# Optimization experiments

Measured on AMD Instinct MI355X. Metric: run time of the kernel, lower is better.

The kernel has to match this reference:

```python
import jax, jax.numpy as jnp
import numpy as np

N = 50000
E = 640000
H = 128

def setup_inputs() -> dict:
    key = jax.random.key(0)
    ks = jax.random.split(key, 12)
    def lin(kw, fan_in, fan_out):
        # torch nn.Linear default init: U(-1/sqrt(fan_in), 1/sqrt(fan_in))
        lim = 1.0 / np.sqrt(fan_in)
        return jax.random.uniform(kw, (fan_in, fan_out), jnp.float32, -lim, lim)
    def bias(kb, fan_in, fan_out):
        lim = 1.0 / np.sqrt(fan_in)
        return jax.random.uniform(kb, (fan_out,), jnp.float32, -lim, lim)
    return {
        "x": jax.random.normal(ks[0], (N, H), jnp.float32),
        "pos": jax.random.normal(ks[1], (N, 3), jnp.float32),
        "edge_index": jax.random.randint(ks[2], (2, E), 0, N, jnp.int64),
        "msg_w1": lin(ks[3], 2 * H + 1, H), "msg_b1": bias(ks[4], 2 * H + 1, H),
        "msg_w2": lin(ks[5], H, H),         "msg_b2": bias(ks[6], H, H),
        "upd_w1": lin(ks[7], 2 * H, H),     "upd_b1": bias(ks[8], 2 * H, H),
        "upd_w2": lin(ks[9], H, H),         "upd_b2": bias(ks[10], H, H),
    }

def reference(x, pos, edge_index, msg_w1, msg_b1, msg_w2, msg_b2,
              upd_w1, upd_b1, upd_w2, upd_b2):
    send, rec = edge_index[0], edge_index[1]
    # pairwise distance per edge: [E]
    dist = jnp.linalg.norm(pos[send] - pos[rec], axis=1)
    # per-edge state: [E, 2H+1]
    state = jnp.concatenate([x[send], x[rec], dist[:, None]], axis=1)
    # message MLP: Linear -> SiLU -> Linear -> SiLU
    h = jax.nn.silu(state @ msg_w1 + msg_b1)
    message = jax.nn.silu(h @ msg_w2 + msg_b2)  # [E, H]
    # scatter-add into receiving nodes: [N, H]
    aggr = jax.ops.segment_sum(message, rec, num_segments=x.shape[0])
    # update MLP: Linear -> SiLU -> Linear
    u = jax.nn.silu(jnp.concatenate([x, aggr], axis=1) @ upd_w1 + upd_b1)
    update = u @ upd_w2 + upd_b2
    return update
```

## Files before the change

### kernel.cpp

```cpp
#include <hip/hip_runtime.h>
#include <math.h>

#define H 128

typedef unsigned short u16;
typedef unsigned int u32;
typedef __attribute__((ext_vector_type(4))) u32 u32x4;
typedef __attribute__((ext_vector_type(8))) __bf16 bf16x8;
typedef __attribute__((ext_vector_type(4))) float f32x4;
typedef __attribute__((ext_vector_type(16))) float f32x16;

union Frag { u32x4 u; bf16x8 b; };

__device__ __forceinline__ u32 pack2(float lo, float hi) {
    union { __bf16 b[2]; u32 u; } v;
    v.b[0] = (__bf16)lo; v.b[1] = (__bf16)hi;
    return v.u;
}
__device__ __forceinline__ float bflo(u32 w) {
    union { u32 i; float f; } v; v.i = w << 16; return v.f;
}
__device__ __forceinline__ float bfhi(u32 w) {
    union { u32 i; float f; } v; v.i = w & 0xffff0000u; return v.f;
}
__device__ __forceinline__ float silu(float v) {
    float e = __expf(-v);
    return v * __builtin_amdgcn_rcpf(1.0f + e);
}
__device__ __forceinline__ bf16x8 f8frag(float4 lo, float4 hi) {
    Frag f;
    f.u = (u32x4){pack2(lo.x, lo.y), pack2(lo.z, lo.w),
                  pack2(hi.x, hi.y), pack2(hi.z, hi.w)};
    return f.b;
}
__device__ __forceinline__ f32x16 mfma(bf16x8 a, bf16x8 b, f32x16 c) {
    return __builtin_amdgcn_mfma_f32_32x32x16_bf16(a, b, c, 0, 0, 0);
}
__device__ __forceinline__ f32x4 mfma16(bf16x8 a, bf16x8 b, f32x4 c) {
    return __builtin_amdgcn_mfma_f32_16x16x32_bf16(a, b, c, 0, 0, 0);
}
#define DPP_RADD(v, ctrl) \
    (v) += __int_as_float(__builtin_amdgcn_update_dpp(0, __float_as_int(v), (ctrl), 0xf, 0xf, 1))

__global__ void prep_kernel(const float* __restrict__ mw1, const float* __restrict__ mb1,
                            const float* __restrict__ mw2, const float* __restrict__ mb2,
                            const float* __restrict__ uw1, const float* __restrict__ ub1,
                            const float* __restrict__ uw2, const float* __restrict__ ub2,
                            u32* __restrict__ ws) {
    int t = blockIdx.x * blockDim.x + threadIdx.x;
    if (t >= 15936) return;
    if (t >= 15872) {
        int i = t - 15872;
        ws[63488 + i] = pack2(mw1[256 * H + 2 * i], mw1[256 * H + 2 * i + 1]);
        return;
    }
    if (t >= 13312) {
        int slot = t - 13312;
        int lane = slot & 63, fb = slot >> 6;
        int kb = fb >> 3, mt = fb & 7;
        int m = mt * 16 + (lane & 15);
        int quad = lane >> 4;
        u32 out[4];
        #pragma unroll
        for (int p = 0; p < 4; ++p) {
            float v[2];
            #pragma unroll
            for (int h = 0; h < 2; ++h) {
                int k = kb * 32 + quad * 8 + p * 2 + h;
                float val = 0.0f;
                if (k < 128)       val = mw2[(size_t)k * H + m];
                else if (k == 128) val = mb2[m];
                v[h] = val;
            }
            out[p] = pack2(v[0], v[1]);
        }
        u32* dst = ws + 53248 + (size_t)slot * 4;
        dst[0] = out[0]; dst[1] = out[1]; dst[2] = out[2]; dst[3] = out[3];
        return;
    }
    const float *W, *s0, *s1;
    int nK, slot, base;
    if (t < 4352)       { W = mw1; s0 = mw1 + 256 * H; s1 = mb1; nK = 256; slot = t;         base = 0;     }
    else if (t < 6656)  { W = mw2; s0 = mb2; s1 = nullptr;       nK = 128; slot = t - 4352;  base = 17408; }
    else if (t < 11008) { W = uw1; s0 = ub1; s1 = nullptr;       nK = 256; slot = t - 6656;  base = 26624; }
    else                { W = uw2; s0 = ub2; s1 = nullptr;       nK = 128; slot = t - 11008; base = 44032; }
    int lane = slot & 63, fb = slot >> 6;
    int ct, kb;
    if (nK == 256) { ct = fb / 17; kb = fb % 17; }
    else           { ct = fb / 9;  kb = fb % 9;  }
    int m = ct * 32 + (lane & 31);
    int q = lane >> 5;
    u32 out[4];
    #pragma unroll
    for (int p = 0; p < 4; ++p) {
        float v[2];
        #pragma unroll
        for (int h = 0; h < 2; ++h) {
            int k = kb * 16 + q * 8 + p * 2 + h;
            float val = 0.0f;
            if (k < nK)            val = W[(size_t)k * H + m];
            else if (k == nK)      val = s0 ? s0[m] : 0.0f;
            else if (k == nK + 1)  val = s1 ? s1[m] : 0.0f;
            v[h] = val;
        }
        out[p] = pack2(v[0], v[1]);
    }
    u32* dst = ws + base + (size_t)slot * 4;
    dst[0] = out[0]; dst[1] = out[1]; dst[2] = out[2]; dst[3] = out[3];
}

__global__ __launch_bounds__(256, 2) void front_kernel(
    const float* __restrict__ x, const u32* __restrict__ ws,
    u32* __restrict__ Pb, u32* __restrict__ Qb, u32* __restrict__ Ub,
    const float* __restrict__ pos, const int* __restrict__ ei,
    int* __restrict__ deg, int2* __restrict__ bucket,
    int N, int E, int nIter, int PQB, int BKB)
{
    const int b = blockIdx.x;
    if (b < 3 * PQB) {
        const int job = b / PQB;
        const int bb = b - job * PQB;
        const int kbBase = (job == 1) ? 8 : 0;
        const u32* wt = (job == 2) ? (ws + 26624) : ws;
        u32* outb = (job == 0) ? Pb : ((job == 1) ? Qb : Ub);

        const int lane = threadIdx.x & 63;
        const int q = lane >> 5, el = lane & 31;
        const int gw  = bb * 4 + (threadIdx.x >> 6);
        const int gws = PQB * 4;

        for (int it = gw; it < nIter; it += gws) {
            const int nA = it * 32 + el;
            const int ncA = (nA < N) ? nA : (N - 1);
            const float* xA = x + (size_t)ncA * H;

            f32x16 acc[4];
            #pragma unroll
            for (int ct = 0; ct < 4; ++ct) acc[ct] = (f32x16)0.0f;

            #pragma unroll
            for (int kb = 0; kb < 8; ++kb) {
                const int f = kb * 16 + q * 8;
                bf16x8 bA = f8frag(*(const float4*)(xA + f), *(const float4*)(xA + f + 4));
                #pragma unroll
                for (int ct = 0; ct < 4; ++ct) {
                    Frag a; a.u = *(const u32x4*)&wt[((size_t)(ct * 17 + kbBase + kb) * 64 + lane) * 4];
                    acc[ct] = mfma(a.b, bA, acc[ct]);
                }
            }
            if (job == 1) {
                Frag bp; bp.u = (u32x4){0, 0, 0, 0};
                if (q == 0) bp.u.x = pack2(0.0f, 1.0f);
                #pragma unroll
                for (int ct = 0; ct < 4; ++ct) {
                    Frag a; a.u = *(const u32x4*)&ws[((size_t)(ct * 17 + 16) * 64 + lane) * 4];
                    acc[ct] = mfma(a.b, bp.b, acc[ct]);
                }
            }
            if (nA < N) {
                u32* prow = outb + (size_t)nA * 64;
                #pragma unroll
                for (int ct = 0; ct < 4; ++ct)
                    #pragma unroll
                    for (int g = 0; g < 4; ++g) {
                        u32 a = pack2(acc[ct][4*g + 0], acc[ct][4*g + 1]);
                        u32 bb2 = pack2(acc[ct][4*g + 2], acc[ct][4*g + 3]);
                        *(uint2*)(prow + ct * 16 + 4 * g + 2 * q) = make_uint2(a, bb2);
                    }
            }
        }
    } else {
        const int bb = b - 3 * PQB;
        for (int e = bb * 256 + (int)threadIdx.x; e < E; e += BKB * 256) {
            const int s = ei[e];
            const int r = ei[E + e];
            const float dx = pos[s*3]   - pos[r*3];
            const float dy = pos[s*3+1] - pos[r*3+1];
            const float dz = pos[s*3+2] - pos[r*3+2];
            const float dist = sqrtf(dx*dx + dy*dy + dz*dz);
            int slot = atomicAdd(&deg[r], 1);
            if (slot < 64) bucket[(size_t)r * 64 + slot] = make_int2(s, __float_as_int(dist));
        }
    }
}

__global__ __launch_bounds__(256, 3) void aggregate_kernel(
    const u32* __restrict__ Pbf, const u32* __restrict__ Qbf,
    const u32* __restrict__ wdp, const u32* __restrict__ ws16,
    const float* __restrict__ mb2,
    const int* __restrict__ deg, const int2* __restrict__ bucket,
    u32* __restrict__ aggrp, int N)
{
    __shared__ u32x4 af[2048];
    __shared__ float b2s[128];
    __shared__ u32x4 wds[16];
    for (int i = threadIdx.x; i < 2048; i += 256) af[i] = ((const u32x4*)ws16)[i];
    for (int i = threadIdx.x; i < 128; i += 256) b2s[i] = mb2[i];
    if (threadIdx.x < 16) wds[threadIdx.x] = ((const u32x4*)wdp)[threadIdx.x];
    __syncthreads();

    const int lane = threadIdx.x & 63;
    const int quad = lane >> 4, col = lane & 15;

    const int gw  = blockIdx.x * 4 + (threadIdx.x >> 6);
    const int gws = gridDim.x * 4;

    for (int n = gw; n < N; n += gws) {
        int dn = deg[n]; dn = (dn > 64) ? 64 : dn;
        const int nt = (dn + 15) >> 4;
        const u32x4* Qrow = (const u32x4*)(Qbf + (size_t)n * 64);

        f32x4 sum[8];
        #pragma unroll
        for (int mt = 0; mt < 8; ++mt) sum[mt] = (f32x4){0.f, 0.f, 0.f, 0.f};

        for (int t = 0; t < nt; ++t) {
            const int eIdx = t * 16 + col;
            const bool valid = eIdx < dn;
            const int eC = valid ? eIdx : (dn - 1);
            const int2 rec = bucket[(size_t)n * 64 + eC];
            const u32x4* Prow = (const u32x4*)(Pbf + (size_t)rec.x * 64);
            const float dist = __int_as_float(rec.y);

            f32x4 acc[8];
            #pragma unroll
            for (int mt = 0; mt < 8; ++mt)
                acc[mt] = *(const f32x4*)&b2s[mt * 16 + quad * 4];

            #pragma unroll 2
            for (int kb = 0; kb < 4; ++kb) {
                const u32x4 pc = Prow[kb * 4 + quad];
                const u32x4 qc = Qrow[kb * 4 + quad];
                const u32x4 wc = wds[kb * 4 + quad];
                const float v0 = silu(bflo(pc.x) + bflo(qc.x) + dist * bflo(wc.x));
                const float v1 = silu(bfhi(pc.x) + bfhi(qc.x) + dist * bfhi(wc.x));
                const float v2 = silu(bflo(pc.y) + bflo(qc.y) + dist * bflo(wc.y));
                const float v3 = silu(bfhi(pc.y) + bfhi(qc.y) + dist * bfhi(wc.y));
                const float v4 = silu(bflo(pc.z) + bflo(qc.z) + dist * bflo(wc.z));
                const float v5 = silu(bfhi(pc.z) + bfhi(qc.z) + dist * bfhi(wc.z));
                const float v6 = silu(bflo(pc.w) + bflo(qc.w) + dist * bflo(wc.w));
                const float v7 = silu(bfhi(pc.w) + bfhi(qc.w) + dist * bfhi(wc.w));
                Frag bf;
                bf.u = (u32x4){pack2(v0, v1), pack2(v2, v3), pack2(v4, v5), pack2(v6, v7)};
                if (!valid) bf.u = (u32x4){0, 0, 0, 0};
                #pragma unroll
                for (int mt = 0; mt < 8; ++mt) {
                    Frag a; a.u = af[(kb * 8 + mt) * 64 + lane];
                    acc[mt] = mfma16(a.b, bf.b, acc[mt]);
                }
            }
            #pragma unroll
            for (int mt = 0; mt < 8; ++mt) {
                sum[mt][0] += valid ? silu(acc[mt][0]) : 0.0f;
                sum[mt][1] += valid ? silu(acc[mt][1]) : 0.0f;
                sum[mt][2] += valid ? silu(acc[mt][2]) : 0.0f;
                sum[mt][3] += valid ? silu(acc[mt][3]) : 0.0f;
            }
        }

        #pragma unroll
        for (int mt = 0; mt < 8; ++mt)
            #pragma unroll
            for (int r = 0; r < 4; ++r) {
                float v = sum[mt][r];
                DPP_RADD(v, 0x128);
                DPP_RADD(v, 0x124);
                DPP_RADD(v, 0x122);
                DPP_RADD(v, 0x121);
                sum[mt][r] = v;
            }
        if (col == 0) {
            u32* orow = aggrp + (size_t)n * 64;
            #pragma unroll
            for (int mt = 0; mt < 8; ++mt) {
                u32 a = pack2(sum[mt][0], sum[mt][1]);
                u32 b = pack2(sum[mt][2], sum[mt][3]);
                *(uint2*)(orow + mt * 8 + quad * 2) = make_uint2(a, b);
            }
        }
    }
}

__global__ __launch_bounds__(256, 2) void node1_slim(
    const u32* __restrict__ aggrp, const u32* __restrict__ Ub,
    const u32* __restrict__ ws, u32* __restrict__ Hb, int N, int nIter)
{
    __shared__ u32 lds[8192];
    const u32* wsl1 = ws + 26624;
    {
        const u32x4* src = (const u32x4*)wsl1;
        u32x4* dst = (u32x4*)lds;
        for (int i = threadIdx.x; i < 2048; i += 256) {
            int ln = i & 63, fb = i >> 6, ct = fb >> 3, kb = fb & 7;
            dst[i] = src[(ct * 17 + 8 + kb) * 64 + ln];
        }
    }
    __syncthreads();

    const int lane = threadIdx.x & 63;
    const int q = lane >> 5, el = lane & 31;
    const int gw  = blockIdx.x * 4 + (threadIdx.x >> 6);
    const int gws = gridDim.x * 4;

    for (int it = gw; it < nIter; it += gws) {
        const int nA = it * 32 + el;
        const int ncA = (nA < N) ? nA : (N - 1);
        const u32* arow = aggrp + (size_t)ncA * 64;
        const u32* Urow = Ub + (size_t)ncA * 64;

        f32x16 acc[4];
        #pragma unroll
        for (int ct = 0; ct < 4; ++ct) acc[ct] = (f32x16)0.0f;

        #pragma unroll
        for (int kb = 0; kb < 8; ++kb) {
            Frag hb; hb.u = *(const u32x4*)&arow[kb * 8 + q * 4];
            #pragma unroll
            for (int ct = 0; ct < 4; ++ct) {
                Frag a; a.u = *(const u32x4*)&lds[((ct * 8 + kb) * 64 + lane) * 4];
                acc[ct] = mfma(a.b, hb.b, acc[ct]);
            }
        }
        {
            Frag bp; bp.u = (u32x4){0,0,0,0};
            if (q == 0) bp.u.x = 0x00003F80u;
            #pragma unroll
            for (int ct = 0; ct < 4; ++ct) {
                Frag a; a.u = *(const u32x4*)&wsl1[((size_t)(ct * 17 + 16) * 64 + lane) * 4];
                acc[ct] = mfma(a.b, bp.b, acc[ct]);
            }
        }
        if (nA < N) {
            u32* hrow = Hb + (size_t)nA * 64;
            #pragma unroll
            for (int ct = 0; ct < 4; ++ct)
                #pragma unroll
                for (int g = 0; g < 4; ++g) {
                    uint2 uv = *(const uint2*)&Urow[ct * 16 + 4 * g + 2 * q];
                    u32 a = pack2(silu(acc[ct][4*g + 0] + bflo(uv.x)),
                                  silu(acc[ct][4*g + 1] + bfhi(uv.x)));
                    u32 b = pack2(silu(acc[ct][4*g + 2] + bflo(uv.y)),
                                  silu(acc[ct][4*g + 3] + bfhi(uv.y)));
                    *(uint2*)(hrow + ct * 16 + 4 * g + 2 * q) = make_uint2(a, b);
                }
        }
    }
}

__global__ __launch_bounds__(256, 2) void node1_full(
    const float* __restrict__ x, const float* __restrict__ aggr,
    const u32* __restrict__ ws, u32* __restrict__ Hb, int N, int nIter)
{
    __shared__ u32 lds[16384];
    const u32* wsl1 = ws + 26624;
    {
        const u32x4* src = (const u32x4*)wsl1;
        u32x4* dst = (u32x4*)lds;
        for (int i = threadIdx.x; i < 4096; i += 256) {
            int ln = i & 63, fb = i >> 6, ct = fb >> 4, kb = fb & 15;
            dst[i] = src[(ct * 17 + kb) * 64 + ln];
        }
    }
    __syncthreads();

    const int lane = threadIdx.x & 63;
    const int q = lane >> 5, el = lane & 31;
    const int gw  = blockIdx.x * 4 + (threadIdx.x >> 6);
    const int gws = gridDim.x * 4;

    for (int it = gw; it < nIter; it += gws) {
        const int nA = it * 32 + el;
        const int ncA = (nA < N) ? nA : (N - 1);
        const float* xA = x + (size_t)ncA * H;
        const float* gA = aggr + (size_t)ncA * H;

        f32x16 acc[4];
        #pragma unroll
        for (int ct = 0; ct < 4; ++ct) acc[ct] = (f32x16)0.0f;

        #pragma unroll
        for (int kb = 0; kb < 16; ++kb) {
            const int f = kb * 16 + q * 8;
            const float* pA = (f < H) ? (xA + f) : (gA + f - H);
            bf16x8 bA = f8frag(*(const float4*)pA, *(const float4*)(pA + 4));
            #pragma unroll
            for (int ct = 0; ct < 4; ++ct) {
                Frag a; a.u = *(const u32x4*)&lds[((ct * 16 + kb) * 64 + lane) * 4];
                acc[ct] = mfma(a.b, bA, acc[ct]);
            }
        }
        {
            Frag bp; bp.u = (u32x4){0,0,0,0};
            if (q == 0) bp.u.x = 0x00003F80u;
            #pragma unroll
            for (int ct = 0; ct < 4; ++ct) {
                Frag a; a.u = *(const u32x4*)&wsl1[((size_t)(ct * 17 + 16) * 64 + lane) * 4];
                acc[ct] = mfma(a.b, bp.b, acc[ct]);
            }
        }
        if (nA < N) {
            u32* hrow = Hb + (size_t)nA * 64;
            #pragma unroll
            for (int ct = 0; ct < 4; ++ct)
                #pragma unroll
                for (int g = 0; g < 4; ++g) {
                    u32 a = pack2(silu(acc[ct][4*g + 0]), silu(acc[ct][4*g + 1]));
                    u32 b = pack2(silu(acc[ct][4*g + 2]), silu(acc[ct][4*g + 3]));
                    *(uint2*)(hrow + ct * 16 + 4 * g + 2 * q) = make_uint2(a, b);
                }
        }
    }
}

__global__ __launch_bounds__(256, 2) void node2_kernel(
    const u32* __restrict__ Hb, const u32* __restrict__ ws,
    float* __restrict__ out, int N, int nIter)
{
    const u32* wsl2 = ws + 44032;
    const int lane = threadIdx.x & 63;
    const int q = lane >> 5, el = lane & 31;
    const int gw  = blockIdx.x * 4 + (threadIdx.x >> 6);
    const int gws = gridDim.x * 4;

    for (int it = gw; it < nIter; it += gws) {
        const int nA = it * 32 + el;
        const int ncA = (nA < N) ? nA : (N - 1);
        const u32* hrow = Hb + (size_t)ncA * 64;

        f32x16 acc[4];
        #pragma unroll
        for (int ct = 0; ct < 4; ++ct) acc[ct] = (f32x16)0.0f;

        #pragma unroll
        for (int kb = 0; kb < 8; ++kb) {
            Frag hb; hb.u = *(const u32x4*)&hrow[kb * 8 + q * 4];
            #pragma unroll
            for (int ct = 0; ct < 4; ++ct) {
                Frag a; a.u = *(const u32x4*)&wsl2[((size_t)(ct * 9 + kb) * 64 + lane) * 4];
                acc[ct] = mfma(a.b, hb.b, acc[ct]);
            }
        }
        {
            Frag bf; bf.u = (u32x4){0,0,0,0};
            if (q == 0) bf.u.x = 0x00003F80u;
            #pragma unroll
            for (int ct = 0; ct < 4; ++ct) {
                Frag a; a.u = *(const u32x4*)&wsl2[((size_t)(ct * 9 + 8) * 64 + lane) * 4];
                acc[ct] = mfma(a.b, bf.b, acc[ct]);
            }
        }
        if (nA < N) {
            float* orow = out + (size_t)nA * H;
            #pragma unroll
            for (int ct = 0; ct < 4; ++ct)
                #pragma unroll
                for (int g = 0; g < 4; ++g) {
                    float4 v = { acc[ct][4*g + 0], acc[ct][4*g + 1],
                                 acc[ct][4*g + 2], acc[ct][4*g + 3] };
                    *(float4*)(orow + ct * 32 + 8 * g + 4 * q) = v;
                }
        }
    }
}

__global__ __launch_bounds__(256, 2) void edge_mfma(
    const float* __restrict__ x, const float* __restrict__ pos,
    const int* __restrict__ ei, const u32* __restrict__ ws,
    float* __restrict__ aggr, int E, int nIter)
{
    __shared__ u32 lds[16384];
    {
        const u32x4* src = (const u32x4*)ws;
        u32x4* dst = (u32x4*)lds;
        for (int i = threadIdx.x; i < 4096; i += 256) {
            int ln = i & 63, fb = i >> 6, ct = fb >> 4, kb = fb & 15;
            dst[i] = src[(ct * 17 + kb) * 64 + ln];
        }
    }
    __syncthreads();
    const u32* wsl1 = ws;
    const u32* wsl2 = ws + 17408;

    const int lane = threadIdx.x & 63;
    const int q = lane >> 5, el = lane & 31;
    const int gw  = blockIdx.x * 4 + (threadIdx.x >> 6);
    const int gws = gridDim.x * 4;

    for (int it = gw; it < nIter; it += gws) {
        const int e0 = it * 64;
        const int sA = ei[e0 + el],      rA = ei[E + e0 + el];
        const int sB = ei[e0 + 32 + el], rB = ei[E + e0 + 32 + el];
        float dA, dB;
        {
            float ax = pos[sA*3] - pos[rA*3], ay = pos[sA*3+1] - pos[rA*3+1], az = pos[sA*3+2] - pos[rA*3+2];
            dA = sqrtf(ax*ax + ay*ay + az*az);
            float bx = pos[sB*3] - pos[rB*3], by = pos[sB*3+1] - pos[rB*3+1], bz = pos[sB*3+2] - pos[rB*3+2];
            dB = sqrtf(bx*bx + by*by + bz*bz);
        }
        const float* xsA = x + (size_t)sA * H; const float* xrA = x + (size_t)rA * H;
        const float* xsB = x + (size_t)sB * H; const float* xrB = x + (size_t)rB * H;

        f32x16 acc[2][4];
        #pragma unroll
        for (int s = 0; s < 2; ++s)
            #pragma unroll
            for (int ct = 0; ct < 4; ++ct) acc[s][ct] = (f32x16)0.0f;

        #pragma unroll
        for (int kb = 0; kb < 16; ++kb) {
            const int f = kb * 16 + q * 8;
            const float* pA = (f < H) ? (xsA + f) : (xrA + f - H);
            const float* pB = (f < H) ? (xsB + f) : (xrB + f - H);
            bf16x8 bA = f8frag(*(const float4*)pA, *(const float4*)(pA + 4));
            bf16x8 bB = f8frag(*(const float4*)pB, *(const float4*)(pB + 4));
            #pragma unroll
            for (int ct = 0; ct < 4; ++ct) {
                Frag a; a.u = *(const u32x4*)&lds[((ct * 16 + kb) * 64 + lane) * 4];
                acc[0][ct] = mfma(a.b, bA, acc[0][ct]);
                acc[1][ct] = mfma(a.b, bB, acc[1][ct]);
            }
        }
        {
            Frag bA, bB;
            bA.u = (u32x4){0,0,0,0}; bB.u = (u32x4){0,0,0,0};
            if (q == 0) { bA.u.x = pack2(dA, 1.0f); bB.u.x = pack2(dB, 1.0f); }
            #pragma unroll
            for (int ct = 0; ct < 4; ++ct) {
                Frag a; a.u = *(const u32x4*)&wsl1[((size_t)(ct * 17 + 16) * 64 + lane) * 4];
                acc[0][ct] = mfma(a.b, bA.b, acc[0][ct]);
                acc[1][ct] = mfma(a.b, bB.b, acc[1][ct]);
            }
        }

        #pragma unroll
        for (int s = 0; s < 2; ++s) {
            const int ridx = s ? rB : rA;
            u32 hp[16][2];
            #pragma unroll
            for (int ct = 0; ct < 4; ++ct)
                #pragma unroll
                for (int g = 0; g < 4; ++g) {
                    hp[ct * 4 + g][0] = pack2(silu(acc[s][ct][4*g + 0]), silu(acc[s][ct][4*g + 1]));
                    hp[ct * 4 + g][1] = pack2(silu(acc[s][ct][4*g + 2]), silu(acc[s][ct][4*g + 3]));
                }

            f32x16 acc2[4];
            #pragma unroll
            for (int ct = 0; ct < 4; ++ct) acc2[ct] = (f32x16)0.0f;

            #pragma unroll
            for (int kb2 = 0; kb2 < 8; ++kb2) {
                const u32 e0v = hp[2 * kb2][0],     e1v = hp[2 * kb2][1];
                const u32 o0v = hp[2 * kb2 + 1][0], o1v = hp[2 * kb2 + 1][1];
                const u32 w0  = q ? o0v : e0v;
                const u32 w1v = q ? o1v : e1v;
                const u32 sv0 = q ? e0v : o0v;
                const u32 sv1 = q ? e1v : o1v;
                u32 r0 = (u32)__shfl((int)sv0, lane ^ 32);
                u32 r1 = (u32)__shfl((int)sv1, lane ^ 32);
                Frag bf;
                if (q == 0) bf.u = (u32x4){w0, w1v, r0, r1};
                else        bf.u = (u32x4){r0, r1, w0, w1v};
                #pragma unroll
                for (int ct2 = 0; ct2 < 4; ++ct2) {
                    Frag a; a.u = *(const u32x4*)&wsl2[((size_t)(ct2 * 9 + kb2) * 64 + lane) * 4];
                    acc2[ct2] = mfma(a.b, bf.b, acc2[ct2]);
                }
            }
            {
                Frag bf; bf.u = (u32x4){0,0,0,0};
                if (q == 0) bf.u.x = 0x00003F80u;
                #pragma unroll
                for (int ct2 = 0; ct2 < 4; ++ct2) {
                    Frag a; a.u = *(const u32x4*)&wsl2[((size_t)(ct2 * 9 + 8) * 64 + lane) * 4];
                    acc2[ct2] = mfma(a.b, bf.b, acc2[ct2]);
                }
            }
            float* arow = aggr + (size_t)ridx * H;
            #pragma unroll
            for (int ct2 = 0; ct2 < 4; ++ct2)
                #pragma unroll
                for (int r = 0; r < 16; ++r) {
                    int m = ct2 * 32 + (r & 3) + 8 * (r >> 2) + 4 * q;
                    atomicAdd(arow + m, silu(acc2[ct2][r]));
                }
        }
    }
}

extern "C" void kernel_launch(void* const* d_in, const int* in_sizes, int n_in,
                              void* d_out, int out_size, void* d_ws, size_t ws_size,
                              hipStream_t stream) {
    const float* x    = (const float*)d_in[0];
    const float* pos  = (const float*)d_in[1];
    const int*   ei   = (const int*)d_in[2];
    const float* mw1  = (const float*)d_in[3];
    const float* mb1  = (const float*)d_in[4];
    const float* mw2  = (const float*)d_in[5];
    const float* mb2  = (const float*)d_in[6];
    const float* uw1  = (const float*)d_in[7];
    const float* ub1  = (const float*)d_in[8];
    const float* uw2  = (const float*)d_in[9];
    const float* ub2  = (const float*)d_in[10];

    const int N = in_sizes[0] / H;
    const int E = in_sizes[2] / 2;

    const size_t FRAGS = 53248 + 10240 + 64;
    const size_t PO = FRAGS;
    const size_t QO = PO + (size_t)N * 64;
    const size_t DG = QO + (size_t)N * 64;
    const size_t BK = DG + (size_t)N;
    const size_t ENDu = BK + (size_t)N * 128;
    const size_t need_bytes = ENDu * 4;

    u32* ws = (u32*)d_ws;
    prep_kernel<<<63, 256, 0, stream>>>(mw1, mb1, mw2, mb2, uw1, ub1, uw2, ub2, ws);

    float* buf = (float*)d_out;
    u32* bufu = (u32*)d_out;
    const int nIter32 = (N + 31) / 32;

    if (ws_size >= need_bytes) {
        u32*   Pb    = ws + PO;
        u32*   Qb    = ws + QO;
        int*   deg   = (int*)(ws + DG);
        int2*  bkt   = (int2*)(ws + BK);
        u32*   aggrp = bufu;
        u32*   Ub    = bufu + (size_t)N * 64;

        hipMemsetAsync(deg, 0, (size_t)N * sizeof(int), stream);

        const int PQB = 392;
        const int BKB = 640;
        front_kernel<<<3 * PQB + BKB, 256, 0, stream>>>(
            x, ws, Pb, Qb, Ub, pos, ei, deg, bkt, N, E, nIter32, PQB, BKB);

        aggregate_kernel<<<768, 256, 0, stream>>>(Pb, Qb, ws + 63488, ws + 53248,
                                                  mb2, deg, bkt, aggrp, N);

        node1_slim<<<512, 256, 0, stream>>>(aggrp, Ub, ws, Pb, N, nIter32);
        node2_kernel<<<512, 256, 0, stream>>>(Pb, ws, buf, N, nIter32);
    } else {
        hipMemsetAsync(buf, 0, (size_t)N * H * sizeof(float), stream);
        edge_mfma<<<512, 256, 0, stream>>>(x, pos, ei, ws, buf, E, E / 64);
        node1_full<<<512, 256, 0, stream>>>(x, buf, ws, ws + PO, N, nIter32);
        node2_kernel<<<512, 256, 0, stream>>>(ws + PO, ws, buf, N, nIter32);
    }
}
```

Before: 332.2 us.

## Software-prefetch next node's degree, bucket entry and first P rows in aggregate

The aggregate kernel now prefetches the degree, first bucket entry and the gathered P row data for the next node a warp will process, overlapping those dependent global loads with the current node's MFMA work. The first 16-edge tile uses the prefetched data through a factored-out helper. To make unconditional prefetch of bucket slot col safe for nodes with few edges, the bucket array is zeroed with an extra memset, which adds a large memory write (N*64*8 bytes) per call. Register pressure also rises from holding prefetched vectors.

```diff
diff --git a/kernel.cpp b/kernel.cpp
--- a/kernel.cpp
+++ b/kernel.cpp
@@ -184,6 +184,48 @@
     }
 }
 
+__device__ __forceinline__ void agg_tile(
+    const u32x4 pc[4], const u32x4* __restrict__ Qrow,
+    const u32x4* __restrict__ wds, const u32x4* __restrict__ af,
+    const float* __restrict__ b2s, float dist, bool valid,
+    int lane, int quad, f32x4 sum[8])
+{
+    f32x4 acc[8];
+    #pragma unroll
+    for (int mt = 0; mt < 8; ++mt)
+        acc[mt] = *(const f32x4*)&b2s[mt * 16 + quad * 4];
+
+    #pragma unroll 2
+    for (int kb = 0; kb < 4; ++kb) {
+        const u32x4 p = pc[kb];
+        const u32x4 qc = Qrow[kb * 4 + quad];
+        const u32x4 wc = wds[kb * 4 + quad];
+        const float v0 = silu(bflo(p.x) + bflo(qc.x) + dist * bflo(wc.x));
+        const float v1 = silu(bfhi(p.x) + bfhi(qc.x) + dist * bfhi(wc.x));
+        const float v2 = silu(bflo(p.y) + bflo(qc.y) + dist * bflo(wc.y));
+        const float v3 = silu(bfhi(p.y) + bfhi(qc.y) + dist * bfhi(wc.y));
+        const float v4 = silu(bflo(p.z) + bflo(qc.z) + dist * bflo(wc.z));
+        const float v5 = silu(bfhi(p.z) + bfhi(qc.z) + dist * bfhi(wc.z));
+        const float v6 = silu(bflo(p.w) + bflo(qc.w) + dist * bflo(wc.w));
+        const float v7 = silu(bfhi(p.w) + bfhi(qc.w) + dist * bfhi(wc.w));
+        Frag bf;
+        bf.u = (u32x4){pack2(v0, v1), pack2(v2, v3), pack2(v4, v5), pack2(v6, v7)};
+        if (!valid) bf.u = (u32x4){0, 0, 0, 0};
+        #pragma unroll
+        for (int mt = 0; mt < 8; ++mt) {
+            Frag a; a.u = af[(kb * 8 + mt) * 64 + lane];
+            acc[mt] = mfma16(a.b, bf.b, acc[mt]);
+        }
+    }
+    #pragma unroll
+    for (int mt = 0; mt < 8; ++mt) {
+        sum[mt][0] += valid ? silu(acc[mt][0]) : 0.0f;
+        sum[mt][1] += valid ? silu(acc[mt][1]) : 0.0f;
+        sum[mt][2] += valid ? silu(acc[mt][2]) : 0.0f;
+        sum[mt][3] += valid ? silu(acc[mt][3]) : 0.0f;
+    }
+}
+
 __global__ __launch_bounds__(256, 3) void aggregate_kernel(
     const u32* __restrict__ Pbf, const u32* __restrict__ Qbf,
     const u32* __restrict__ wdp, const u32* __restrict__ ws16,
@@ -205,57 +247,58 @@
     const int gw  = blockIdx.x * 4 + (threadIdx.x >> 6);
     const int gws = gridDim.x * 4;
 
-    for (int n = gw; n < N; n += gws) {
-        int dn = deg[n]; dn = (dn > 64) ? 64 : dn;
+    int n = gw;
+    int dn_pf = 0;
+    int2 rec_pf = make_int2(0, 0);
+    u32x4 pc_pf[4];
+    #pragma unroll
+    for (int kb = 0; kb < 4; ++kb) pc_pf[kb] = (u32x4){0, 0, 0, 0};
+    if (n < N) {
+        dn_pf  = deg[n];
+        rec_pf = bucket[(size_t)n * 64 + col];
+        const u32x4* Pr = (const u32x4*)(Pbf + (size_t)rec_pf.x * 64);
+        #pragma unroll
+        for (int kb = 0; kb < 4; ++kb) pc_pf[kb] = Pr[kb * 4 + quad];
+    }
+
+    for (; n < N; n += gws) {
+        int dn = dn_pf; dn = (dn > 64) ? 64 : dn;
         const int nt = (dn + 15) >> 4;
+        const float dist0 = __int_as_float(rec_pf.y);
+        u32x4 pc0[4];
+        #pragma unroll
+        for (int kb = 0; kb < 4; ++kb) pc0[kb] = pc_pf[kb];
+
+        const int nn = n + gws;
+        if (nn < N) {
+            dn_pf  = deg[nn];
+            rec_pf = bucket[(size_t)nn * 64 + col];
+        }
+
         const u32x4* Qrow = (const u32x4*)(Qbf + (size_t)n * 64);
 
         f32x4 sum[8];
         #pragma unroll
         for (int mt = 0; mt < 8; ++mt) sum[mt] = (f32x4){0.f, 0.f, 0.f, 0.f};
 
-        for (int t = 0; t < nt; ++t) {
+        agg_tile(pc0, Qrow, wds, af, b2s, dist0, col < dn, lane, quad, sum);
+
+        for (int t = 1; t < nt; ++t) {
             const int eIdx = t * 16 + col;
             const bool valid = eIdx < dn;
             const int eC = valid ? eIdx : (dn - 1);
             const int2 rec = bucket[(size_t)n * 64 + eC];
-            const u32x4* Prow = (const u32x4*)(Pbf + (size_t)rec.x * 64);
-            const float dist = __int_as_float(rec.y);
-
-            f32x4 acc[8];
-            #pragma unroll
-            for (int mt = 0; mt < 8; ++mt)
-                acc[mt] = *(const f32x4*)&b2s[mt * 16 + quad * 4];
-
-            #pragma unroll 2
-            for (int kb = 0; kb < 4; ++kb) {
-                const u32x4 pc = Prow[kb * 4 + quad];
-                const u32x4 qc = Qrow[kb * 4 + quad];
-                const u32x4 wc = wds[kb * 4 + quad];
-                const float v0 = silu(bflo(pc.x) + bflo(qc.x) + dist * bflo(wc.x));
-                const float v1 = silu(bfhi(pc.x) + bfhi(qc.x) + dist * bfhi(wc.x));
-                const float v2 = silu(bflo(pc.y) + bflo(qc.y) + dist * bflo(wc.y));
-                const float v3 = silu(bfhi(pc.y) + bfhi(qc.y) + dist * bfhi(wc.y));
-                const float v4 = silu(bflo(pc.z) + bflo(qc.z) + dist * bflo(wc.z));
-                const float v5 = silu(bfhi(pc.z) + bfhi(qc.z) + dist * bfhi(wc.z));
-                const float v6 = silu(bflo(pc.w) + bflo(qc.w) + dist * bflo(wc.w));
-                const float v7 = silu(bfhi(pc.w) + bfhi(qc.w) + dist * bfhi(wc.w));
-                Frag bf;
-                bf.u = (u32x4){pack2(v0, v1), pack2(v2, v3), pack2(v4, v5), pack2(v6, v7)};
-                if (!valid) bf.u = (u32x4){0, 0, 0, 0};
-                #pragma unroll
-                for (int mt = 0; mt < 8; ++mt) {
-                    Frag a; a.u = af[(kb * 8 + mt) * 64 + lane];
-                    acc[mt] = mfma16(a.b, bf.b, acc[mt]);
-                }
-            }
-            #pragma unroll
-            for (int mt = 0; mt < 8; ++mt) {
-                sum[mt][0] += valid ? silu(acc[mt][0]) : 0.0f;
-                sum[mt][1] += valid ? silu(acc[mt][1]) : 0.0f;
-                sum[mt][2] += valid ? silu(acc[mt][2]) : 0.0f;
-                sum[mt][3] += valid ? silu(acc[mt][3]) : 0.0f;
-            }
+            const u32x4* Pr = (const u32x4*)(Pbf + (size_t)rec.x * 64);
+            u32x4 pc[4];
+            #pragma unroll
+            for (int kb = 0; kb < 4; ++kb) pc[kb] = Pr[kb * 4 + quad];
+            agg_tile(pc, Qrow, wds, af, b2s, __int_as_float(rec.y), valid, lane, quad, sum);
+        }
+
+        if (nn < N) {
+            const u32x4* Pr = (const u32x4*)(Pbf + (size_t)rec_pf.x * 64);
+            #pragma unroll
+            for (int kb = 0; kb < 4; ++kb) pc_pf[kb] = Pr[kb * 4 + quad];
         }
 
         #pragma unroll
@@ -630,6 +673,7 @@
         u32*   Ub    = bufu + (size_t)N * 64;
 
         hipMemsetAsync(deg, 0, (size_t)N * sizeof(int), stream);
+        hipMemsetAsync(bkt, 0, (size_t)N * 64 * sizeof(int2), stream);
 
         const int PQB = 392;
         const int BKB = 640;
```

Measured after the change: 358.8 us. 1.08x slower.
